# Performance work log

Measured on AMD Instinct MI355X. Metric: run time of the kernel, lower is better.

The kernel has to match this reference:

```python
import jax, jax.numpy as jnp
import numpy as np

B, N = 256, 512
DIM_GRAPH = 256
DIM_DESC = 256
RANK = 64


def setup_inputs() -> dict:
    key = jax.random.key(0)
    ks = jax.random.split(key, 6)
    tokns_k = jax.random.normal(ks[0], (B, DIM_DESC), dtype=jnp.float32)
    H_pad = jax.random.normal(ks[1], (B, N, DIM_GRAPH), dtype=jnp.float32)
    mask = jax.random.randint(ks[2], (B, N), 0, 2).astype(bool)
    mask = mask.at[:, 0].set(True)  # ensure at least one valid node per graph
    # Linear weights, torch convention: y = x @ W.T
    Wq = jax.random.normal(ks[3], (RANK, DIM_DESC), dtype=jnp.float32) / np.sqrt(DIM_DESC)
    Wk = jax.random.normal(ks[4], (RANK, DIM_GRAPH), dtype=jnp.float32) / np.sqrt(DIM_GRAPH)
    Wv = jax.random.normal(ks[5], (DIM_DESC, DIM_GRAPH), dtype=jnp.float32) / np.sqrt(DIM_GRAPH)
    log_scale = jnp.zeros((1,), dtype=jnp.float32)
    return {"tokns_k": tokns_k, "H_pad": H_pad, "mask": mask,
            "Wq": Wq, "Wk": Wk, "Wv": Wv, "log_scale": log_scale}


def reference(tokns_k, H_pad, mask, Wq, Wk, Wv, log_scale):
    q = tokns_k @ Wq.T                                  # [B, r]
    k = jnp.einsum('bnd,rd->bnr', H_pad, Wk)            # [B, N, r]
    scale = jnp.maximum(jnp.exp(log_scale), 0.1)        # clamp(min=0.1)
    scores = jnp.einsum('br,bnr->bn', q, k) / scale     # [B, N]
    neg_inf = jnp.float32(-jnp.inf)
    scores = jnp.where(mask, scores, neg_inf)
    alpha = jax.nn.softmax(scores, axis=-1)             # [B, N]
    v = jnp.einsum('bnd,ed->bne', H_pad, Wv)            # [B, N, dim_desc]
    ctx_k = jnp.einsum('bn,bne->be', alpha, v)          # [B, dim_desc]
    return (alpha, ctx_k)
```

## Files before the change

kernel.cpp:

```cpp
#include <hip/hip_runtime.h>

constexpr int Bc = 256;
constexpr int Nc = 512;
constexpr int Dc = 256;
constexpr int Rc = 64;
constexpr int SPLIT = 4;
constexpr int ROWS = Nc / SPLIT;
constexpr int NSTEP = ROWS / 16;

typedef float f4 __attribute__((ext_vector_type(4)));

constexpr size_t WS_P = 0;
constexpr size_t WS_L = WS_P + (size_t)Bc * Dc;
constexpr size_t WS_H = WS_L + (size_t)Bc * SPLIT;
constexpr size_t WS_FLOATS = WS_H + (size_t)Bc * SPLIT * Dc;

__global__ __launch_bounds__(256) void k0_precompute_p(
    const float* __restrict__ tokns_k, const float* __restrict__ Wq,
    const float* __restrict__ Wk, float* __restrict__ ws)
{
    const int b = blockIdx.x;
    const int t = threadIdx.x;
    const int wave = t >> 6, lane = t & 63, g = lane >> 4, l16 = lane & 15;

    __shared__ float q_s[Rc];

    #pragma unroll
    for (int step = 0; step < 4; ++step) {
        const int r = wave * 16 + step * 4 + g;
        float acc = 0.0f;
        #pragma unroll
        for (int j = 0; j < 4; ++j) {
            const float4 tk = *(const float4*)(tokns_k + b * Dc + l16 * 4 + j * 64);
            const float4 wq = *(const float4*)(Wq + r * Dc + l16 * 4 + j * 64);
            acc += tk.x * wq.x + tk.y * wq.y + tk.z * wq.z + tk.w * wq.w;
        }
        #pragma unroll
        for (int off = 1; off < 16; off <<= 1) acc += __shfl_xor(acc, off);
        if (l16 == 0) q_s[r] = acc;
    }
    __syncthreads();

    float acc = 0.0f;
    #pragma unroll 8
    for (int r = 0; r < Rc; ++r) acc += q_s[r] * Wk[r * Dc + t];
    ws[WS_P + (size_t)b * Dc + t] = acc;
}

__global__ __launch_bounds__(256) void k1_stream(
    const float* __restrict__ H_pad, const int* __restrict__ mask,
    const float* __restrict__ log_scale, float* __restrict__ ws,
    float* __restrict__ out)
{
    const int s = blockIdx.x;
    const int b = blockIdx.y;
    const int t = threadIdx.x;
    const int wave = t >> 6, lane = t & 63, g = lane >> 4, l16 = lane & 15;
    const int n0 = s * ROWS;
    const int team = wave * 4 + g;

    __shared__ __align__(16) float hm[16][Dc];
    __shared__ float l_s[16];
    __shared__ float scores_s[ROWS];
    __shared__ int   mask_s[ROWS];

    if (t < ROWS) mask_s[t] = mask[b * Nc + n0 + t];

    const float inv_scale = 1.0f / fmaxf(__expf(log_scale[0]), 0.1f);

    const float* __restrict__ pb = ws + WS_P + (size_t)b * Dc;
    float4 p4[4];
    #pragma unroll
    for (int j = 0; j < 4; ++j) p4[j] = *(const float4*)(pb + l16 * 4 + j * 64);
    __syncthreads();

    int actbits = 0;
    #pragma unroll
    for (int k = 0; k < NSTEP; ++k)
        actbits |= (mask_s[k * 16 + team] != 0) ? (1 << k) : 0;

    const float* __restrict__ Hb = H_pad + ((size_t)b * Nc + n0) * Dc;
    float  l_acc = 0.0f;
    float4 h4[4];
    #pragma unroll
    for (int j = 0; j < 4; ++j) h4[j] = make_float4(0.f, 0.f, 0.f, 0.f);

    auto LOADROW = [&](f4 (&x)[4], int nr, bool act) {
        if (act) {
            const float* __restrict__ row = Hb + nr * Dc + l16 * 4;
            #pragma unroll
            for (int j = 0; j < 4; ++j)
                x[j] = __builtin_nontemporal_load((const f4*)(row + j * 64));
        }
    };
    auto PROCROW = [&](const f4 (&x)[4], int nr, bool act) {
        if (!act) {
            if (l16 == 0) scores_s[nr] = -1e30f;
            return;
        }
        float s0 = x[0][0] * p4[0].x + x[0][1] * p4[0].y + x[0][2] * p4[0].z + x[0][3] * p4[0].w;
        float s1 = x[1][0] * p4[1].x + x[1][1] * p4[1].y + x[1][2] * p4[1].z + x[1][3] * p4[1].w;
        float s2 = x[2][0] * p4[2].x + x[2][1] * p4[2].y + x[2][2] * p4[2].z + x[2][3] * p4[2].w;
        float s3 = x[3][0] * p4[3].x + x[3][1] * p4[3].y + x[3][2] * p4[3].z + x[3][3] * p4[3].w;
        float sc = (s0 + s1) + (s2 + s3);
        #pragma unroll
        for (int off = 1; off < 16; off <<= 1) sc += __shfl_xor(sc, off);
        sc *= inv_scale;
        if (l16 == 0) scores_s[nr] = sc;

        const float pn = __expf(sc);
        l_acc += pn;
        #pragma unroll
        for (int j = 0; j < 4; ++j) {
            h4[j].x = fmaf(pn, x[j][0], h4[j].x);
            h4[j].y = fmaf(pn, x[j][1], h4[j].y);
            h4[j].z = fmaf(pn, x[j][2], h4[j].z);
            h4[j].w = fmaf(pn, x[j][3], h4[j].w);
        }
    };

    f4 xa[4], xb[4];
    LOADROW(xa, team, (actbits >> 0) & 1);
    #pragma unroll
    for (int it = 0; it < NSTEP / 2; ++it) {
        const int nrA = it * 32 + team;
        const int nrB = nrA + 16;
        const bool actA = (actbits >> (2 * it)) & 1;
        const bool actB = (actbits >> (2 * it + 1)) & 1;
        LOADROW(xb, nrB, actB);
        PROCROW(xa, nrA, actA);
        if (it + 1 < NSTEP / 2)
            LOADROW(xa, nrA + 32, (actbits >> (2 * it + 2)) & 1);
        PROCROW(xb, nrB, actB);
    }

    #pragma unroll
    for (int j = 0; j < 4; ++j) *(float4*)(&hm[team][l16 * 4 + j * 64]) = h4[j];
    if (l16 == 0) l_s[team] = l_acc;
    __syncthreads();

    if (t < ROWS) out[b * Nc + n0 + t] = scores_s[t];
    float hsum = 0.0f;
    #pragma unroll
    for (int p = 0; p < 16; ++p) hsum += hm[p][t];
    ws[WS_H + ((size_t)b * SPLIT + s) * Dc + t] = hsum;
    if (t == 0) {
        float L = 0.0f;
        #pragma unroll
        for (int p = 0; p < 16; ++p) L += l_s[p];
        ws[WS_L + (size_t)b * SPLIT + s] = L;
    }
}

__global__ __launch_bounds__(256) void k2_merge(
    const float* __restrict__ Wv, const float* __restrict__ ws,
    float* __restrict__ out)
{
    const int b = blockIdx.x;
    const int t = threadIdx.x;
    const int wave = t >> 6, lane = t & 63, g = lane >> 4, l16 = lane & 15;

    __shared__ __align__(16) float hbar[Dc];

    float L = 0.0f;
    #pragma unroll
    for (int s = 0; s < SPLIT; ++s) L += ws[WS_L + (size_t)b * SPLIT + s];
    const float invL = 1.0f / L;

    float hacc = 0.0f;
    #pragma unroll
    for (int s = 0; s < SPLIT; ++s) hacc += ws[WS_H + ((size_t)b * SPLIT + s) * Dc + t];
    hbar[t] = hacc * invL;

    #pragma unroll
    for (int i = 0; i < Nc / 256; ++i) {
        const int idx = b * Nc + i * 256 + t;
        out[idx] = __expf(out[idx]) * invL;
    }
    __syncthreads();

    float4 hb4[4];
    #pragma unroll
    for (int j = 0; j < 4; ++j) hb4[j] = *(const float4*)(hbar + l16 * 4 + j * 64);
    float* __restrict__ ctx_out = out + (size_t)Bc * Nc + b * Dc;
    #pragma unroll
    for (int step = 0; step < 16; ++step) {
        const int e = step * 16 + wave * 4 + g;
        float acc = 0.0f;
        #pragma unroll
        for (int j = 0; j < 4; ++j) {
            const float4 wv = *(const float4*)(Wv + e * Dc + l16 * 4 + j * 64);
            acc += wv.x * hb4[j].x + wv.y * hb4[j].y + wv.z * hb4[j].z + wv.w * hb4[j].w;
        }
        #pragma unroll
        for (int off = 1; off < 16; off <<= 1) acc += __shfl_xor(acc, off);
        if (l16 == 0) ctx_out[e] = acc;
    }
}

constexpr int FNT = 512;
constexpr int FNW = FNT / 64;
constexpr int FNPW = Nc / FNW;

__global__ __launch_bounds__(FNT) void fba_fallback(
    const float* __restrict__ tokns_k, const float* __restrict__ H_pad,
    const int* __restrict__ mask, const float* __restrict__ Wq,
    const float* __restrict__ Wk, const float* __restrict__ Wv,
    const float* __restrict__ log_scale, float* __restrict__ out)
{
    const int b = blockIdx.x, t = threadIdx.x;
    const int wave = t >> 6, lane = t & 63;

    __shared__ __align__(16) float q_s[Rc];
    __shared__ __align__(16) float p_s[Dc];
    __shared__ __align__(16) float scores_s[Nc];
    __shared__ __align__(16) float hmerge[FNW][Dc];
    __shared__ float l_s[FNW];
    __shared__ __align__(16) float hbar[Dc];
    __shared__ int mask_s[Nc];

    const float inv_scale = 1.0f / fmaxf(__expf(log_scale[0]), 0.1f);

    const float4 tok4 = *(const float4*)(tokns_k + b * Dc + lane * 4);
    #pragma unroll
    for (int i = 0; i < Rc / FNW; ++i) {
        const int r = wave * (Rc / FNW) + i;
        const float4 w4 = *(const float4*)(Wq + r * Dc + lane * 4);
        float s = w4.x * tok4.x + w4.y * tok4.y + w4.z * tok4.z + w4.w * tok4.w;
        #pragma unroll
        for (int off = 32; off >= 1; off >>= 1) s += __shfl_xor(s, off);
        if (lane == 0) q_s[r] = s;
    }
    mask_s[t] = mask[b * Nc + t];
    mask_s[t + FNT] = mask[b * Nc + t + FNT];
    __syncthreads();

    if (t < Dc) {
        float acc = 0.0f;
        #pragma unroll 8
        for (int r = 0; r < Rc; ++r) acc += q_s[r] * Wk[r * Dc + t];
        p_s[t] = acc;
    }
    __syncthreads();

    const float4 p4 = *(const float4*)(p_s + lane * 4);
    const float* Hb = H_pad + (size_t)b * Nc * Dc;
    float l_acc = 0.0f;
    float4 h4 = make_float4(0.f, 0.f, 0.f, 0.f);

    for (int i = 0; i < FNPW; ++i) {
        const int n = wave * FNPW + i;
        const float4 x4 = *(const float4*)(Hb + n * Dc + lane * 4);
        float s = x4.x * p4.x + x4.y * p4.y + x4.z * p4.z + x4.w * p4.w;
        #pragma unroll
        for (int off = 32; off >= 1; off >>= 1) s += __shfl_xor(s, off);
        s *= inv_scale;
        if (mask_s[n] == 0) s = -1e30f;
        if (lane == 0) scores_s[n] = s;
        const float pn = __expf(s);
        l_acc += pn;
        h4.x = fmaf(pn, x4.x, h4.x); h4.y = fmaf(pn, x4.y, h4.y);
        h4.z = fmaf(pn, x4.z, h4.z); h4.w = fmaf(pn, x4.w, h4.w);
    }

    if (lane == 0) l_s[wave] = l_acc;
    *(float4*)(&hmerge[wave][lane * 4]) = h4;
    __syncthreads();

    float L = 0.0f;
    #pragma unroll
    for (int w = 0; w < FNW; ++w) L += l_s[w];
    const float invL = 1.0f / L;

    if (t < Dc) {
        float acc = 0.0f;
        #pragma unroll
        for (int w = 0; w < FNW; ++w) acc += hmerge[w][t];
        hbar[t] = acc * invL;
    }
    out[b * Nc + t] = __expf(scores_s[t]) * invL;
    out[b * Nc + t + FNT] = __expf(scores_s[t + FNT]) * invL;
    __syncthreads();

    const float4 hb4 = *(const float4*)(hbar + lane * 4);
    float* ctx_out = out + (size_t)Bc * Nc + b * Dc;
    #pragma unroll
    for (int i = 0; i < Dc / FNW; ++i) {
        const int e = wave * (Dc / FNW) + i;
        const float4 w4 = *(const float4*)(Wv + e * Dc + lane * 4);
        float s = w4.x * hb4.x + w4.y * hb4.y + w4.z * hb4.z + w4.w * hb4.w;
        #pragma unroll
        for (int off = 32; off >= 1; off >>= 1) s += __shfl_xor(s, off);
        if (lane == 0) ctx_out[e] = s;
    }
}

extern "C" void kernel_launch(void* const* d_in, const int* in_sizes, int n_in,
                              void* d_out, int out_size, void* d_ws, size_t ws_size,
                              hipStream_t stream) {
    const float* tokns_k   = (const float*)d_in[0];
    const float* H_pad     = (const float*)d_in[1];
    const int*   mask      = (const int*)d_in[2];
    const float* Wq        = (const float*)d_in[3];
    const float* Wk        = (const float*)d_in[4];
    const float* Wv        = (const float*)d_in[5];
    const float* log_scale = (const float*)d_in[6];
    float* out = (float*)d_out;

    if (ws_size >= WS_FLOATS * sizeof(float)) {
        float* ws = (float*)d_ws;
        k0_precompute_p<<<Bc, 256, 0, stream>>>(tokns_k, Wq, Wk, ws);
        dim3 grid1(SPLIT, Bc);
        k1_stream<<<grid1, 256, 0, stream>>>(H_pad, mask, log_scale, ws, out);
        k2_merge<<<Bc, 256, 0, stream>>>(Wv, ws, out);
    } else {
        fba_fallback<<<Bc, FNT, 0, stream>>>(tokns_k, H_pad, mask, Wq, Wk, Wv,
                                             log_scale, out);
    }
}
```

Before: 202.4 us.

## Fuse three-kernel split pipeline into one 512-thread block per batch

```diff
diff --git a/kernel.cpp b/kernel.cpp
--- a/kernel.cpp
+++ b/kernel.cpp
@@ -4,30 +4,39 @@
 constexpr int Nc = 512;
 constexpr int Dc = 256;
 constexpr int Rc = 64;
-constexpr int SPLIT = 4;
-constexpr int ROWS = Nc / SPLIT;
-constexpr int NSTEP = ROWS / 16;
+
+constexpr int NT    = 512;
+constexpr int NTEAM = 32;
+constexpr int NSTEP = Nc / NTEAM;
 
 typedef float f4 __attribute__((ext_vector_type(4)));
 
-constexpr size_t WS_P = 0;
-constexpr size_t WS_L = WS_P + (size_t)Bc * Dc;
-constexpr size_t WS_H = WS_L + (size_t)Bc * SPLIT;
-constexpr size_t WS_FLOATS = WS_H + (size_t)Bc * SPLIT * Dc;
-
-__global__ __launch_bounds__(256) void k0_precompute_p(
-    const float* __restrict__ tokns_k, const float* __restrict__ Wq,
-    const float* __restrict__ Wk, float* __restrict__ ws)
+__global__ __launch_bounds__(NT) void fba_fused(
+    const float* __restrict__ tokns_k, const float* __restrict__ H_pad,
+    const int* __restrict__ mask, const float* __restrict__ Wq,
+    const float* __restrict__ Wk, const float* __restrict__ Wv,
+    const float* __restrict__ log_scale, float* __restrict__ out)
 {
     const int b = blockIdx.x;
     const int t = threadIdx.x;
     const int wave = t >> 6, lane = t & 63, g = lane >> 4, l16 = lane & 15;
+    const int team = wave * 4 + g;
 
     __shared__ float q_s[Rc];
+    __shared__ __align__(16) float p_s[Dc];
+    __shared__ __align__(16) float hm[NTEAM][Dc];
+    __shared__ float l_s[NTEAM];
+    __shared__ float scores_s[Nc];
+    __shared__ __align__(16) float hbar[Dc];
+    __shared__ int   mask_s[Nc];
+
+    mask_s[t] = mask[b * Nc + t];
+
+    const float inv_scale = 1.0f / fmaxf(__expf(log_scale[0]), 0.1f);
 
     #pragma unroll
-    for (int step = 0; step < 4; ++step) {
-        const int r = wave * 16 + step * 4 + g;
+    for (int step = 0; step < 2; ++step) {
+        const int r = step * NTEAM + team;
         float acc = 0.0f;
         #pragma unroll
         for (int j = 0; j < 4; ++j) {
@@ -41,45 +50,24 @@
     }
     __syncthreads();
 
-    float acc = 0.0f;
-    #pragma unroll 8
-    for (int r = 0; r < Rc; ++r) acc += q_s[r] * Wk[r * Dc + t];
-    ws[WS_P + (size_t)b * Dc + t] = acc;
-}
+    if (t < Dc) {
+        float acc = 0.0f;
+        #pragma unroll 16
+        for (int r = 0; r < Rc; ++r) acc += q_s[r] * Wk[r * Dc + t];
+        p_s[t] = acc;
+    }
+    __syncthreads();
 
-__global__ __launch_bounds__(256) void k1_stream(
-    const float* __restrict__ H_pad, const int* __restrict__ mask,
-    const float* __restrict__ log_scale, float* __restrict__ ws,
-    float* __restrict__ out)
-{
-    const int s = blockIdx.x;
-    const int b = blockIdx.y;
-    const int t = threadIdx.x;
-    const int wave = t >> 6, lane = t & 63, g = lane >> 4, l16 = lane & 15;
-    const int n0 = s * ROWS;
-    const int team = wave * 4 + g;
-
-    __shared__ __align__(16) float hm[16][Dc];
-    __shared__ float l_s[16];
-    __shared__ float scores_s[ROWS];
-    __shared__ int   mask_s[ROWS];
-
-    if (t < ROWS) mask_s[t] = mask[b * Nc + n0 + t];
-
-    const float inv_scale = 1.0f / fmaxf(__expf(log_scale[0]), 0.1f);
-
-    const float* __restrict__ pb = ws + WS_P + (size_t)b * Dc;
     float4 p4[4];
     #pragma unroll
-    for (int j = 0; j < 4; ++j) p4[j] = *(const float4*)(pb + l16 * 4 + j * 64);
-    __syncthreads();
+    for (int j = 0; j < 4; ++j) p4[j] = *(const float4*)(p_s + l16 * 4 + j * 64);
 
     int actbits = 0;
     #pragma unroll
     for (int k = 0; k < NSTEP; ++k)
-        actbits |= (mask_s[k * 16 + team] != 0) ? (1 << k) : 0;
+        actbits |= (mask_s[k * NTEAM + team] != 0) ? (1 << k) : 0;
 
-    const float* __restrict__ Hb = H_pad + ((size_t)b * Nc + n0) * Dc;
+    const float* __restrict__ Hb = H_pad + (size_t)b * Nc * Dc;
     float  l_acc = 0.0f;
     float4 h4[4];
     #pragma unroll
@@ -123,14 +111,14 @@
     LOADROW(xa, team, (actbits >> 0) & 1);
     #pragma unroll
     for (int it = 0; it < NSTEP / 2; ++it) {
-        const int nrA = it * 32 + team;
-        const int nrB = nrA + 16;
+        const int nrA = it * (2 * NTEAM) + team;
+        const int nrB = nrA + NTEAM;
         const bool actA = (actbits >> (2 * it)) & 1;
         const bool actB = (actbits >> (2 * it + 1)) & 1;
         LOADROW(xb, nrB, actB);
         PROCROW(xa, nrA, actA);
         if (it + 1 < NSTEP / 2)
-            LOADROW(xa, nrA + 32, (actbits >> (2 * it + 2)) & 1);
+            LOADROW(xa, nrA + 2 * NTEAM, (actbits >> (2 * it + 2)) & 1);
         PROCROW(xb, nrB, actB);
     }
 
@@ -139,44 +127,18 @@
     if (l16 == 0) l_s[team] = l_acc;
     __syncthreads();
 
-    if (t < ROWS) out[b * Nc + n0 + t] = scores_s[t];
-    float hsum = 0.0f;
-    #pragma unroll
-    for (int p = 0; p < 16; ++p) hsum += hm[p][t];
-    ws[WS_H + ((size_t)b * SPLIT + s) * Dc + t] = hsum;
-    if (t == 0) {
-        float L = 0.0f;
-        #pragma unroll
-        for (int p = 0; p < 16; ++p) L += l_s[p];
-        ws[WS_L + (size_t)b * SPLIT + s] = L;
-    }
-}
-
-__global__ __launch_bounds__(256) void k2_merge(
-    const float* __restrict__ Wv, const float* __restrict__ ws,
-    float* __restrict__ out)
-{
-    const int b = blockIdx.x;
-    const int t = threadIdx.x;
-    const int wave = t >> 6, lane = t & 63, g = lane >> 4, l16 = lane & 15;
-
-    __shared__ __align__(16) float hbar[Dc];
-
     float L = 0.0f;
     #pragma unroll
-    for (int s = 0; s < SPLIT; ++s) L += ws[WS_L + (size_t)b * SPLIT + s];
+    for (int p = 0; p < NTEAM; ++p) L += l_s[p];
     const float invL = 1.0f / L;
 
-    float hacc = 0.0f;
-    #pragma unroll
-    for (int s = 0; s < SPLIT; ++s) hacc += ws[WS_H + ((size_t)b * SPLIT + s) * Dc + t];
-    hbar[t] = hacc * invL;
-
-    #pragma unroll
-    for (int i = 0; i < Nc / 256; ++i) {
-        const int idx = b * Nc + i * 256 + t;
-        out[idx] = __expf(out[idx]) * invL;
+    if (t < Dc) {
+        float hsum = 0.0f;
+        #pragma unroll
+        for (int p = 0; p < NTEAM; ++p) hsum += hm[p][t];
+        hbar[t] = hsum * invL;
     }
+    out[b * Nc + t] = __expf(scores_s[t]) * invL;
     __syncthreads();
 
     float4 hb4[4];
@@ -184,8 +146,8 @@
     for (int j = 0; j < 4; ++j) hb4[j] = *(const float4*)(hbar + l16 * 4 + j * 64);
     float* __restrict__ ctx_out = out + (size_t)Bc * Nc + b * Dc;
     #pragma unroll
-    for (int step = 0; step < 16; ++step) {
-        const int e = step * 16 + wave * 4 + g;
+    for (int step = 0; step < Dc / NTEAM; ++step) {
+        const int e = step * NTEAM + team;
         float acc = 0.0f;
         #pragma unroll
         for (int j = 0; j < 4; ++j) {
@@ -195,103 +157,6 @@
         #pragma unroll
         for (int off = 1; off < 16; off <<= 1) acc += __shfl_xor(acc, off);
         if (l16 == 0) ctx_out[e] = acc;
-    }
-}
-
-constexpr int FNT = 512;
-constexpr int FNW = FNT / 64;
-constexpr int FNPW = Nc / FNW;
-
-__global__ __launch_bounds__(FNT) void fba_fallback(
-    const float* __restrict__ tokns_k, const float* __restrict__ H_pad,
-    const int* __restrict__ mask, const float* __restrict__ Wq,
-    const float* __restrict__ Wk, const float* __restrict__ Wv,
-    const float* __restrict__ log_scale, float* __restrict__ out)
-{
-    const int b = blockIdx.x, t = threadIdx.x;
-    const int wave = t >> 6, lane = t & 63;
-
-    __shared__ __align__(16) float q_s[Rc];
-    __shared__ __align__(16) float p_s[Dc];
-    __shared__ __align__(16) float scores_s[Nc];
-    __shared__ __align__(16) float hmerge[FNW][Dc];
-    __shared__ float l_s[FNW];
-    __shared__ __align__(16) float hbar[Dc];
-    __shared__ int mask_s[Nc];
-
-    const float inv_scale = 1.0f / fmaxf(__expf(log_scale[0]), 0.1f);
-
-    const float4 tok4 = *(const float4*)(tokns_k + b * Dc + lane * 4);
-    #pragma unroll
-    for (int i = 0; i < Rc / FNW; ++i) {
-        const int r = wave * (Rc / FNW) + i;
-        const float4 w4 = *(const float4*)(Wq + r * Dc + lane * 4);
-        float s = w4.x * tok4.x + w4.y * tok4.y + w4.z * tok4.z + w4.w * tok4.w;
-        #pragma unroll
-        for (int off = 32; off >= 1; off >>= 1) s += __shfl_xor(s, off);
-        if (lane == 0) q_s[r] = s;
-    }
-    mask_s[t] = mask[b * Nc + t];
-    mask_s[t + FNT] = mask[b * Nc + t + FNT];
-    __syncthreads();
-
-    if (t < Dc) {
-        float acc = 0.0f;
-        #pragma unroll 8
-        for (int r = 0; r < Rc; ++r) acc += q_s[r] * Wk[r * Dc + t];
-        p_s[t] = acc;
-    }
-    __syncthreads();
-
-    const float4 p4 = *(const float4*)(p_s + lane * 4);
-    const float* Hb = H_pad + (size_t)b * Nc * Dc;
-    float l_acc = 0.0f;
-    float4 h4 = make_float4(0.f, 0.f, 0.f, 0.f);
-
-    for (int i = 0; i < FNPW; ++i) {
-        const int n = wave * FNPW + i;
-        const float4 x4 = *(const float4*)(Hb + n * Dc + lane * 4);
-        float s = x4.x * p4.x + x4.y * p4.y + x4.z * p4.z + x4.w * p4.w;
-        #pragma unroll
-        for (int off = 32; off >= 1; off >>= 1) s += __shfl_xor(s, off);
-        s *= inv_scale;
-        if (mask_s[n] == 0) s = -1e30f;
-        if (lane == 0) scores_s[n] = s;
-        const float pn = __expf(s);
-        l_acc += pn;
-        h4.x = fmaf(pn, x4.x, h4.x); h4.y = fmaf(pn, x4.y, h4.y);
-        h4.z = fmaf(pn, x4.z, h4.z); h4.w = fmaf(pn, x4.w, h4.w);
-    }
-
-    if (lane == 0) l_s[wave] = l_acc;
-    *(float4*)(&hmerge[wave][lane * 4]) = h4;
-    __syncthreads();
-
-    float L = 0.0f;
-    #pragma unroll
-    for (int w = 0; w < FNW; ++w) L += l_s[w];
-    const float invL = 1.0f / L;
-
-    if (t < Dc) {
-        float acc = 0.0f;
-        #pragma unroll
-        for (int w = 0; w < FNW; ++w) acc += hmerge[w][t];
-        hbar[t] = acc * invL;
-    }
-    out[b * Nc + t] = __expf(scores_s[t]) * invL;
-    out[b * Nc + t + FNT] = __expf(scores_s[t + FNT]) * invL;
-    __syncthreads();
-
-    const float4 hb4 = *(const float4*)(hbar + lane * 4);
-    float* ctx_out = out + (size_t)Bc * Nc + b * Dc;
-    #pragma unroll
-    for (int i = 0; i < Dc / FNW; ++i) {
-        const int e = wave * (Dc / FNW) + i;
-        const float4 w4 = *(const float4*)(Wv + e * Dc + lane * 4);
-        float s = w4.x * hb4.x + w4.y * hb4.y + w4.z * hb4.z + w4.w * hb4.w;
-        #pragma unroll
-        for (int off = 32; off >= 1; off >>= 1) s += __shfl_xor(s, off);
-        if (lane == 0) ctx_out[e] = s;
     }
 }
 
@@ -306,15 +171,8 @@
     const float* Wv        = (const float*)d_in[5];
     const float* log_scale = (const float*)d_in[6];
     float* out = (float*)d_out;
+    (void)d_ws; (void)ws_size;
 
-    if (ws_size >= WS_FLOATS * sizeof(float)) {
-        float* ws = (float*)d_ws;
-        k0_precompute_p<<<Bc, 256, 0, stream>>>(tokns_k, Wq, Wk, ws);
-        dim3 grid1(SPLIT, Bc);
-        k1_stream<<<grid1, 256, 0, stream>>>(H_pad, mask, log_scale, ws, out);
-        k2_merge<<<Bc, 256, 0, stream>>>(Wv, ws, out);
-    } else {
-        fba_fallback<<<Bc, FNT, 0, stream>>>(tokns_k, H_pad, mask, Wq, Wk, Wv,
-                                             log_scale, out);
-    }
+    fba_fused<<<Bc, NT, 0, stream>>>(tokns_k, H_pad, mask, Wq, Wk, Wv,
+                                     log_scale, out);
 }
```

After: 192.2 us. 1.05x faster.
